# Kernel optimization log

Measured on AMD Instinct MI355X. Metric: run time of the kernel, lower is better.

Reference implementation:

```python
import jax, jax.numpy as jnp
import numpy as np
import math

D_MODEL = 1024
NUM_HEADS = 16
D_K = D_MODEL // NUM_HEADS
THETA = 10000.0
BATCH = 2
SEQ = 2048


def setup_inputs() -> dict:
    key = jax.random.key(0)
    k = jax.random.split(key, 6)
    scale = 1.0 / math.sqrt(D_MODEL)
    in_features = jax.random.normal(k[0], (BATCH, SEQ, D_MODEL), dtype=jnp.float32)
    token_positions = jnp.sort(
        jax.random.randint(k[1], (BATCH, SEQ), 0, SEQ), axis=-1
    ).astype(jnp.int32)
    q_proj_weight = jax.random.normal(k[2], (D_MODEL, D_MODEL), dtype=jnp.float32) * scale
    k_proj_weight = jax.random.normal(k[3], (D_MODEL, D_MODEL), dtype=jnp.float32) * scale
    v_proj_weight = jax.random.normal(k[4], (D_MODEL, D_MODEL), dtype=jnp.float32) * scale
    o_proj_weight = jax.random.normal(k[5], (D_MODEL, D_MODEL), dtype=jnp.float32) * scale
    return {
        "in_features": in_features,
        "token_positions": token_positions,
        "q_proj_weight": q_proj_weight,
        "k_proj_weight": k_proj_weight,
        "v_proj_weight": v_proj_weight,
        "o_proj_weight": o_proj_weight,
    }


def _apply_rope(x, positions):
    # x: [b, h, s, d_k]; positions: [b, s]
    freqs = 1.0 / (THETA ** (jnp.arange(0, D_K, 2, dtype=jnp.float32) / D_K))  # [d_k/2]
    angles = positions[:, None, :, None].astype(jnp.float32) * freqs  # [b,1,s,d_k/2]
    cos, sin = jnp.cos(angles), jnp.sin(angles)
    x1 = x[..., 0::2]
    x2 = x[..., 1::2]
    x1r = x1 * cos - x2 * sin
    x2r = x1 * sin + x2 * cos
    # interleave pairs back: stack on new last axis then flatten
    return jnp.stack([x1r, x2r], axis=-1).reshape(x.shape)


def reference(in_features, token_positions, q_proj_weight, k_proj_weight,
              v_proj_weight, o_proj_weight):
    b, s, _ = in_features.shape
    Q = jnp.einsum('bsi,di->bsd', in_features, q_proj_weight)
    K = jnp.einsum('bsi,di->bsd', in_features, k_proj_weight)
    V = jnp.einsum('bsi,di->bsd', in_features, v_proj_weight)
    # split heads: [b, h, s, d_k]
    def split(x):
        return x.reshape(b, s, NUM_HEADS, D_K).transpose(0, 2, 1, 3)
    Q, K, V = split(Q), split(K), split(V)
    Q = _apply_rope(Q, token_positions)
    K = _apply_rope(K, token_positions)
    scores = jnp.einsum('bhqd,bhkd->bhqk', Q, K) / math.sqrt(D_K)
    causal = jnp.tril(jnp.ones((s, s), dtype=bool))  # allowed positions
    scores = jnp.where(causal[None, None], scores, -jnp.inf)
    weights = jax.nn.softmax(scores, axis=-1)
    head_out = jnp.einsum('bhqk,bhkd->bhqd', weights, V)
    combined = head_out.transpose(0, 2, 1, 3).reshape(b, s, D_MODEL)
    return jnp.einsum('bsd,od->bso', combined, o_proj_weight)
```

## Files before the change

kernel.cpp:

```cpp
#include <hip/hip_runtime.h>
#include <hip/hip_bf16.h>
#include <stdint.h>

#define DMODEL 1024
#define NH 16
#define DKH 64
#define BB 2
#define SS 2048
#define MTOT (BB*SS)

#define TP 136

using f32x4  = __attribute__((ext_vector_type(4))) float;
using bf16x8 = __attribute__((ext_vector_type(8))) __bf16;

#define GLL(g, l) __builtin_amdgcn_global_load_lds( \
    (const __attribute__((address_space(1))) unsigned int*)(g), \
    (__attribute__((address_space(3))) unsigned int*)(l), 16, 0, 0)

__device__ __forceinline__ unsigned short f2bf(float f) {
  union { float f; uint32_t u; } v; v.f = f;
  uint32_t r = v.u + 0x7FFFu + ((v.u >> 16) & 1u);
  return (unsigned short)(r >> 16);
}

__global__ __launch_bounds__(256) void cvt_all(
    const float* __restrict__ X,
    const float* __restrict__ w0, const float* __restrict__ w1,
    const float* __restrict__ w2, const float* __restrict__ w3,
    unsigned short* __restrict__ Xb,
    unsigned short* __restrict__ Wb)
{
  const int bid = blockIdx.x;
  const float* src;
  unsigned short* dst;
  int i;
  if (bid < 2048) {
    src = X; dst = Xb; i = bid * 256 + threadIdx.x;
  } else {
    int t = bid - 2048;
    int z = t >> 9;
    src = (z == 0) ? w0 : (z == 1) ? w1 : (z == 2) ? w2 : w3;
    dst = Wb + (size_t)z * DMODEL * DMODEL;
    i = (t & 511) * 256 + threadIdx.x;
  }
  const float4* s4 = (const float4*)src;
  float4 a = s4[2*i], b = s4[2*i+1];
  uint4 o;
  o.x = (uint32_t)f2bf(a.x) | ((uint32_t)f2bf(a.y) << 16);
  o.y = (uint32_t)f2bf(a.z) | ((uint32_t)f2bf(a.w) << 16);
  o.z = (uint32_t)f2bf(b.x) | ((uint32_t)f2bf(b.y) << 16);
  o.w = (uint32_t)f2bf(b.z) | ((uint32_t)f2bf(b.w) << 16);
  *(uint4*)(dst + (size_t)i * 8) = o;
}

template<int MI, int NI, int KU>
__device__ __forceinline__ void gemm_pipe(
    const unsigned short* __restrict__ A,
    const unsigned short* __restrict__ Bw,
    int m0, int n0, int K,
    unsigned short* As, unsigned short* Bs,
    f32x4 (&acc)[MI][NI])
{
  const int BKT = 32 * KU;
  const int BMl = MI * 32;
  const int BNl = NI * 32;
  const int tid = threadIdx.x;
  const int lane = tid & 63;
  const int w = tid >> 6;
  const int wr = w >> 1, wc = w & 1;
  const int lrow = lane & 15;
  const int g = lane >> 4;

  const f32x4 fzero = {0.f, 0.f, 0.f, 0.f};
  #pragma unroll
  for (int i = 0; i < MI; ++i)
    #pragma unroll
    for (int j = 0; j < NI; ++j)
      acc[i][j] = fzero;

  const int nk = K / BKT;

  const unsigned short* aSrc[(MI * KU) / 2];
  const unsigned short* bSrc[(NI * KU) / 2];
  int aLds[(MI * KU) / 2], bLds[(NI * KU) / 2];
  #pragma unroll
  for (int c = 0; c < (MI * KU) / 2; ++c) {
    int i = tid + c * 256;
    int row, sc;
    if constexpr (KU == 1) { row = i >> 2; sc = (i & 3) ^ ((row >> 1) & 3); }
    else                   { row = i >> 3; sc = (i & 7) ^ (row & 7); }
    aSrc[c] = A + (size_t)(m0 + row) * K + sc * 8;
    aLds[c] = i * 8;
  }
  #pragma unroll
  for (int c = 0; c < (NI * KU) / 2; ++c) {
    int i = tid + c * 256;
    int row, sc;
    if constexpr (KU == 1) { row = i >> 2; sc = (i & 3) ^ ((row >> 1) & 3); }
    else                   { row = i >> 3; sc = (i & 7) ^ (row & 7); }
    bSrc[c] = Bw + (size_t)(n0 + row) * K + sc * 8;
    bLds[c] = i * 8;
  }
  int aOff[KU][MI], bOff[KU][NI];
  #pragma unroll
  for (int u = 0; u < KU; ++u) {
    #pragma unroll
    for (int mi = 0; mi < MI; ++mi) {
      int row = wr * (MI * 16) + mi * 16 + lrow;
      int ch = (KU == 1) ? (g ^ ((row >> 1) & 3)) : ((g + 4 * u) ^ (row & 7));
      aOff[u][mi] = row * BKT + ch * 8;
    }
    #pragma unroll
    for (int ni = 0; ni < NI; ++ni) {
      int row = wc * (NI * 16) + ni * 16 + lrow;
      int ch = (KU == 1) ? (g ^ ((row >> 1) & 3)) : ((g + 4 * u) ^ (row & 7));
      bOff[u][ni] = row * BKT + ch * 8;
    }
  }

  auto STAGE = [&](int k0, int buf) {
    #pragma unroll
    for (int c = 0; c < (MI * KU) / 2; ++c)
      GLL(aSrc[c] + k0, As + buf * (BMl * BKT) + aLds[c]);
    #pragma unroll
    for (int c = 0; c < (NI * KU) / 2; ++c)
      GLL(bSrc[c] + k0, Bs + buf * (BNl * BKT) + bLds[c]);
  };

  STAGE(0, 0);
  __syncthreads();
  for (int t = 0; t < nk; ++t) {
    const int cur = t & 1;
    if (t + 1 < nk) STAGE((t + 1) * BKT, cur ^ 1);

    const unsigned short* Ab = As + cur * (BMl * BKT);
    const unsigned short* Bb = Bs + cur * (BNl * BKT);
    #pragma unroll
    for (int u = 0; u < KU; ++u) {
      bf16x8 af[MI], bfr[NI];
      #pragma unroll
      for (int mi = 0; mi < MI; ++mi)
        af[mi] = *(const bf16x8*)(Ab + aOff[u][mi]);
      #pragma unroll
      for (int ni = 0; ni < NI; ++ni)
        bfr[ni] = *(const bf16x8*)(Bb + bOff[u][ni]);
      #pragma unroll
      for (int mi = 0; mi < MI; ++mi)
        #pragma unroll
        for (int ni = 0; ni < NI; ++ni)
          acc[mi][ni] = __builtin_amdgcn_mfma_f32_16x16x32_bf16(af[mi], bfr[ni], acc[mi][ni], 0, 0, 0);
    }

    __syncthreads();
  }
}

__global__ __launch_bounds__(256) void gemm_qkv(
    const unsigned short* __restrict__ Xb,
    const unsigned short* __restrict__ Wf,
    const int* __restrict__ tpos,
    unsigned short* __restrict__ Qh,
    unsigned short* __restrict__ Kh,
    unsigned short* __restrict__ Vt)
{
  __shared__ __align__(16) unsigned char smraw[65536];
  unsigned short* sm = (unsigned short*)smraw;
  unsigned short* As = sm;
  unsigned short* Bs = sm + 2 * 128 * 64;

  const int m0 = blockIdx.x * 128;
  const int n0 = blockIdx.y * 128;
  const int z  = n0 >> 10;
  const int nloc = n0 & 1023;

  f32x4 acc[4][4];
  gemm_pipe<4, 4, 2>(Xb, Wf, m0, n0, DMODEL, As, Bs, acc);

  const int tid  = threadIdx.x;
  const int lane = tid & 63;
  const int w    = tid >> 6;
  const int wr   = w >> 1, wc = w & 1;
  const int cb   = lane & 15, rb = (lane >> 4) * 4;

  if (z < 2) {
    #pragma unroll
    for (int mi = 0; mi < 4; ++mi)
      #pragma unroll
      for (int ni = 0; ni < 4; ++ni)
        #pragma unroll
        for (int r = 0; r < 4; ++r)
          sm[(wr * 64 + mi * 16 + rb + r) * TP + wc * 64 + ni * 16 + cb] = f2bf(acc[mi][ni][r]);
  } else {
    #pragma unroll
    for (int mi = 0; mi < 4; ++mi)
      #pragma unroll
      for (int ni = 0; ni < 4; ++ni)
        #pragma unroll
        for (int r = 0; r < 4; ++r)
          sm[(wc * 64 + ni * 16 + cb) * TP + wr * 64 + mi * 16 + rb + r] = f2bf(acc[mi][ni][r]);
  }
  __syncthreads();

  const int b = m0 >> 11;
  const float l2t = 13.28771237954945f / 32.0f;
  const float qsc = (z == 0) ? 0.18033688011112042f : 1.0f;

  if (z < 2) {
    unsigned short* dst = (z == 0) ? Qh : Kh;
    #pragma unroll
    for (int p = 0; p < 8; ++p) {
      const int m_l = p * 16 + (tid >> 4);
      const int ck  = tid & 15;
      bf16x8 vals = *(const bf16x8*)(sm + m_l * TP + ck * 8);
      const int m = m0 + m_l, s = m & (SS - 1);
      const int pos = tpos[m];
      const int n = nloc + ck * 8, h = n >> 6, dh = n & 63;
      union { unsigned short u[8]; uint4 v; } ov;
      #pragma unroll
      for (int e = 0; e < 4; ++e) {
        float x1 = (float)vals[2 * e], x2 = (float)vals[2 * e + 1];
        int j = (dh >> 1) + e;
        float ang = (float)pos * exp2f(-(float)j * l2t);
        float sn, cs;
        __sincosf(ang, &sn, &cs);
        sn *= qsc; cs *= qsc;
        ov.u[2 * e]     = f2bf(x1 * cs - x2 * sn);
        ov.u[2 * e + 1] = f2bf(x1 * sn + x2 * cs);
      }
      *(uint4*)(dst + ((size_t)(b * NH + h) * SS + s) * DKH + dh) = ov.v;
    }
  } else {
    #pragma unroll
    for (int p = 0; p < 8; ++p) {
      const int n_l = p * 16 + (tid >> 4);
      const int ck  = tid & 15;
      bf16x8 vals = *(const bf16x8*)(sm + n_l * TP + ck * 8);
      const int n = nloc + n_l, h = n >> 6, dh = n & 63;
      const int m = m0 + ck * 8, s = m & (SS - 1);
      *(bf16x8*)(Vt + ((size_t)(b * NH + h) * DKH + dh) * SS + s) = vals;
    }
  }
}

__global__ __launch_bounds__(256) void attn(
    const unsigned short* __restrict__ Qh,
    const unsigned short* __restrict__ Kh,
    const unsigned short* __restrict__ Vt,
    unsigned short* __restrict__ comb)
{
  __shared__ unsigned short Ks[2][128 * 64];
  __shared__ unsigned short Vs[2][64 * 128];
  __shared__ unsigned short Ps[4][32 * 64];

  const int idx = blockIdx.x;
  const int x = idx & 7;
  const int o = idx >> 3;
  const int bh = x * 4 + (o & 3);
  const int j = o >> 2;
  const int qt = ((j & 7) << 1) | (j >> 3);

  const int tid = threadIdx.x, lane = tid & 63, w = tid >> 6;
  const int lc = lane & 15, lh = lane >> 4;

  const unsigned short* kb = Kh + (size_t)bh * SS * DKH;
  const unsigned short* vb = Vt + (size_t)bh * DKH * SS;
  const int b = bh >> 4, h = bh & 15;
  const f32x4 fzero = {0.f, 0.f, 0.f, 0.f};
  const int Q0 = qt * 128;

  auto STAGE = [&](int t, int buf) {
    const int kv0 = t * 128;
    #pragma unroll
    for (int c = 0; c < 4; ++c) {
      int i = tid + c * 256;
      int row = i >> 3, pc = i & 7;
      int sc = pc ^ (row & 7);
      GLL(kb + (size_t)(kv0 + row) * DKH + sc * 8, &Ks[buf][i * 8]);
    }
    #pragma unroll
    for (int c = 0; c < 4; ++c) {
      int i = tid + c * 256;
      int row = i >> 4, cc = i & 15;
      int sc = cc ^ (row & 7);
      GLL(vb + (size_t)row * SS + kv0 + sc * 8, &Vs[buf][i * 8]);
    }
  };

  bf16x8 qf[2][2];
  #pragma unroll
  for (int qg = 0; qg < 2; ++qg) {
    const unsigned short* Qb = Qh + ((size_t)bh * SS + Q0 + w * 32 + qg * 16 + lc) * DKH;
    qf[qg][0] = *(const bf16x8*)(Qb + lh * 8);
    qf[qg][1] = *(const bf16x8*)(Qb + lh * 8 + 32);
  }

  f32x4 oacc[2][4];
  #pragma unroll
  for (int qg = 0; qg < 2; ++qg)
    #pragma unroll
    for (int i = 0; i < 4; ++i) oacc[qg][i] = fzero;
  float lsum[2] = {0.f, 0.f};
  unsigned short* psw = &Ps[w][0];

  auto QK = [&](int cur, int hh, f32x4 (&sacc)[2][4]) {
    __builtin_amdgcn_s_setprio(1);
    #pragma unroll
    for (int nf = 0; nf < 4; ++nf) {
      const int row = hh * 64 + nf * 16 + lc;
      bf16x8 kf0 = *(const bf16x8*)(&Ks[cur][row * 64 + ((lh) ^ (row & 7)) * 8]);
      bf16x8 kf1 = *(const bf16x8*)(&Ks[cur][row * 64 + ((lh + 4) ^ (row & 7)) * 8]);
      #pragma unroll
      for (int qg = 0; qg < 2; ++qg) {
        sacc[qg][nf] = __builtin_amdgcn_mfma_f32_16x16x32_bf16(kf0, qf[qg][0], fzero, 0, 0, 0);
        sacc[qg][nf] = __builtin_amdgcn_mfma_f32_16x16x32_bf16(kf1, qf[qg][1], sacc[qg][nf], 0, 0, 0);
      }
    }
    __builtin_amdgcn_s_setprio(0);
  };

  auto SM = [&](f32x4 (&sacc)[2][4], bool domask, int t, int hh) {
    #pragma unroll
    for (int qg = 0; qg < 2; ++qg) {
      float sv[4][4];
      if (domask) {
        const int kv0 = t * 128 + hh * 64;
        const int qlane = Q0 + w * 32 + qg * 16 + lc;
        #pragma unroll
        for (int nf = 0; nf < 4; ++nf)
          #pragma unroll
          for (int r = 0; r < 4; ++r) {
            float x2 = sacc[qg][nf][r];
            if ((kv0 + nf * 16 + lh * 4 + r) > qlane) x2 = -1e30f;
            sv[nf][r] = x2;
          }
      } else {
        #pragma unroll
        for (int nf = 0; nf < 4; ++nf)
          #pragma unroll
          for (int r = 0; r < 4; ++r)
            sv[nf][r] = sacc[qg][nf][r];
      }
      float rs = 0.f;
      #pragma unroll
      for (int nf = 0; nf < 4; ++nf)
        #pragma unroll
        for (int r = 0; r < 4; ++r) {
          float p = exp2f(sv[nf][r]);
          sv[nf][r] = p;
          rs += p;
        }
      lsum[qg] += rs;
      #pragma unroll
      for (int nf = 0; nf < 4; ++nf) {
        uint32_t u0, u1;
        asm("v_cvt_pk_bf16_f32 %0, %1, %2" : "=v"(u0) : "v"(sv[nf][0]), "v"(sv[nf][1]));
        asm("v_cvt_pk_bf16_f32 %0, %1, %2" : "=v"(u1) : "v"(sv[nf][2]), "v"(sv[nf][3]));
        int swz = (nf * 2 + (lh >> 1)) ^ (lc & 7);
        uint32_t* p = (uint32_t*)&psw[(qg * 16 + lc) * 64 + swz * 8 + (lh & 1) * 4];
        p[0] = u0; p[1] = u1;
      }
    }
  };

  auto PV = [&](int cur, int hh) {
    __builtin_amdgcn_s_setprio(1);
    #pragma unroll
    for (int c = 0; c < 2; ++c) {
      bf16x8 pf[2];
      #pragma unroll
      for (int qg = 0; qg < 2; ++qg)
        pf[qg] = *(const bf16x8*)(&psw[(qg * 16 + lc) * 64 + ((c * 4 + lh) ^ (lc & 7)) * 8]);
      #pragma unroll
      for (int df = 0; df < 4; ++df) {
        const int row = df * 16 + lc;
        bf16x8 vf = *(const bf16x8*)(&Vs[cur][row * 128 + ((hh * 8 + c * 4 + lh) ^ (row & 7)) * 8]);
        #pragma unroll
        for (int qg = 0; qg < 2; ++qg)
          oacc[qg][df] = __builtin_amdgcn_mfma_f32_16x16x32_bf16(pf[qg], vf, oacc[qg][df], 0, 0, 0);
      }
    }
    __builtin_amdgcn_s_setprio(0);
  };

  STAGE(0, 0);
  for (int t = 0; t < qt; ++t) {
    const int cur = t & 1;
    asm volatile("s_waitcnt vmcnt(0)" ::: "memory");
    __builtin_amdgcn_s_barrier();
    f32x4 sA[2][4], sB[2][4];
    QK(cur, 0, sA);
    QK(cur, 1, sB);
    STAGE(t + 1, cur ^ 1);
    SM(sA, false, t, 0);
    PV(cur, 0);
    SM(sB, false, t, 1);
    PV(cur, 1);
  }
  {
    const int cur = qt & 1;
    asm volatile("s_waitcnt vmcnt(0)" ::: "memory");
    __builtin_amdgcn_s_barrier();
    f32x4 sA[2][4], sB[2][4];
    QK(cur, 0, sA);
    QK(cur, 1, sB);
    SM(sA, true, qt, 0);
    PV(cur, 0);
    SM(sB, true, qt, 1);
    PV(cur, 1);
  }

  #pragma unroll
  for (int qg = 0; qg < 2; ++qg) {
    float ls0 = lsum[qg];
    ls0 += __shfl_xor(ls0, 16);
    ls0 += __shfl_xor(ls0, 32);
    #pragma unroll
    for (int r = 0; r < 4; ++r) {
      float ls = __shfl(ls0, lh * 4 + r);
      float inv = 1.f / ls;
      const int q = Q0 + w * 32 + qg * 16 + lh * 4 + r;
      #pragma unroll
      for (int df = 0; df < 4; ++df) {
        const int d = h * 64 + df * 16 + lc;
        comb[((size_t)(b * SS + q)) * DMODEL + d] = f2bf(oacc[qg][df][r] * inv);
      }
    }
  }
}

__global__ __launch_bounds__(256) void gemm_out(
    const unsigned short* __restrict__ Cb,
    const unsigned short* __restrict__ Wob,
    float* __restrict__ out)
{
  __shared__ __align__(16) unsigned char smraw[49152];
  unsigned short* As = (unsigned short*)smraw;
  unsigned short* Bs = (unsigned short*)smraw + 2 * 128 * 64;
  float* smf = (float*)smraw;

  const int m0 = blockIdx.x * 128, n0 = blockIdx.y * 64;
  f32x4 acc[4][2];
  gemm_pipe<4, 2, 2>(Cb, Wob, m0, n0, DMODEL, As, Bs, acc);

  const int tid  = threadIdx.x;
  const int lane = tid & 63;
  const int w    = tid >> 6;
  const int wr   = w >> 1, wc = w & 1;
  const int cb   = lane & 15, rb = (lane >> 4) * 4;

  #pragma unroll
  for (int mi = 0; mi < 4; ++mi)
    #pragma unroll
    for (int ni = 0; ni < 2; ++ni)
      #pragma unroll
      for (int r = 0; r < 4; ++r)
        smf[(wr * 64 + mi * 16 + rb + r) * 68 + wc * 32 + ni * 16 + cb] = acc[mi][ni][r];
  __syncthreads();

  #pragma unroll
  for (int p = 0; p < 8; ++p) {
    const int row = p * 16 + (tid >> 4);
    const int ck  = tid & 15;
    float4 vv = *(const float4*)(smf + row * 68 + ck * 4);
    *(float4*)(out + (size_t)(m0 + row) * DMODEL + n0 + ck * 4) = vv;
  }
}

extern "C" void kernel_launch(void* const* d_in, const int* in_sizes, int n_in,
                              void* d_out, int out_size, void* d_ws, size_t ws_size,
                              hipStream_t stream) {
  (void)in_sizes; (void)n_in; (void)out_size; (void)ws_size;
  const float* X    = (const float*)d_in[0];
  const int*   tpos = (const int*)d_in[1];
  const float* Wq   = (const float*)d_in[2];
  const float* Wk   = (const float*)d_in[3];
  const float* Wv   = (const float*)d_in[4];
  const float* Wo   = (const float*)d_in[5];
  float* out = (float*)d_out;

  uint8_t* ws = (uint8_t*)d_ws;
  const size_t SZ_X = (size_t)MTOT * DMODEL * 2;
  const size_t SZ_W = (size_t)DMODEL * DMODEL * 2;
  const size_t SZ_H = (size_t)BB * NH * SS * DKH * 2;
  unsigned short* Xb   = (unsigned short*)(ws);
  unsigned short* Wqb  = (unsigned short*)(ws + SZ_X);
  unsigned short* Wob  = (unsigned short*)(ws + SZ_X + 3 * SZ_W);
  unsigned short* Qh   = (unsigned short*)(ws + SZ_X + 4 * SZ_W);
  unsigned short* Kh   = (unsigned short*)(ws + SZ_X + 4 * SZ_W + SZ_H);
  unsigned short* Vt   = (unsigned short*)(ws + SZ_X + 4 * SZ_W + 2 * SZ_H);
  unsigned short* comb = Xb;

  cvt_all<<<dim3(4096), dim3(256), 0, stream>>>(X, Wq, Wk, Wv, Wo, Xb, Wqb);

  gemm_qkv<<<dim3(MTOT / 128, 24), dim3(256), 0, stream>>>(Xb, Wqb, tpos, Qh, Kh, Vt);
  attn<<<dim3(512), dim3(256), 0, stream>>>(Qh, Kh, Vt, comb);
  gemm_out<<<dim3(MTOT / 128, 16), dim3(256), 0, stream>>>(comb, Wob, out);
}
```

Before: 116.7 us.

## Split attention query tile across eight waves and reorder query-tile scheduling

The attention kernel now runs 512 threads per block. Each of the eight waves handles 16 query rows instead of 32, which halves per-wave accumulator registers and raises the number of waves sharing each staged K/V tile. The query-tile ordering changes from an interleaved permutation to a pattern that pairs short and long causal tiles (j for the first 8, 23-j after). The trade is more waves contending for LDS bandwidth, and each K fragment read from LDS now feeds only one MFMA rather than two.

```diff
diff --git a/kernel.cpp b/kernel.cpp
--- a/kernel.cpp
+++ b/kernel.cpp
@@ -243,7 +243,7 @@
   }
 }
 
-__global__ __launch_bounds__(256) void attn(
+__global__ __launch_bounds__(512) void attn(
     const unsigned short* __restrict__ Qh,
     const unsigned short* __restrict__ Kh,
     const unsigned short* __restrict__ Vt,
@@ -251,17 +251,18 @@
 {
   __shared__ unsigned short Ks[2][128 * 64];
   __shared__ unsigned short Vs[2][64 * 128];
-  __shared__ unsigned short Ps[4][32 * 64];
+  __shared__ unsigned short Ps[8][16 * 64];
 
   const int idx = blockIdx.x;
   const int x = idx & 7;
   const int o = idx >> 3;
   const int bh = x * 4 + (o & 3);
   const int j = o >> 2;
-  const int qt = ((j & 7) << 1) | (j >> 3);
+  const int qt = (j < 8) ? j : 23 - j;
 
   const int tid = threadIdx.x, lane = tid & 63, w = tid >> 6;
   const int lc = lane & 15, lh = lane >> 4;
+  const int wq = w >> 1, qg = w & 1;
 
   const unsigned short* kb = Kh + (size_t)bh * SS * DKH;
   const unsigned short* vb = Vt + (size_t)bh * DKH * SS;
@@ -272,94 +273,82 @@
   auto STAGE = [&](int t, int buf) {
     const int kv0 = t * 128;
     #pragma unroll
-    for (int c = 0; c < 4; ++c) {
-      int i = tid + c * 256;
+    for (int c = 0; c < 2; ++c) {
+      int i = tid + c * 512;
       int row = i >> 3, pc = i & 7;
       int sc = pc ^ (row & 7);
       GLL(kb + (size_t)(kv0 + row) * DKH + sc * 8, &Ks[buf][i * 8]);
     }
     #pragma unroll
-    for (int c = 0; c < 4; ++c) {
-      int i = tid + c * 256;
+    for (int c = 0; c < 2; ++c) {
+      int i = tid + c * 512;
       int row = i >> 4, cc = i & 15;
       int sc = cc ^ (row & 7);
       GLL(vb + (size_t)row * SS + kv0 + sc * 8, &Vs[buf][i * 8]);
     }
   };
 
-  bf16x8 qf[2][2];
-  #pragma unroll
-  for (int qg = 0; qg < 2; ++qg) {
-    const unsigned short* Qb = Qh + ((size_t)bh * SS + Q0 + w * 32 + qg * 16 + lc) * DKH;
-    qf[qg][0] = *(const bf16x8*)(Qb + lh * 8);
-    qf[qg][1] = *(const bf16x8*)(Qb + lh * 8 + 32);
-  }
-
-  f32x4 oacc[2][4];
-  #pragma unroll
-  for (int qg = 0; qg < 2; ++qg)
-    #pragma unroll
-    for (int i = 0; i < 4; ++i) oacc[qg][i] = fzero;
-  float lsum[2] = {0.f, 0.f};
+  const unsigned short* Qb = Qh + ((size_t)bh * SS + Q0 + wq * 32 + qg * 16 + lc) * DKH;
+  bf16x8 qf0 = *(const bf16x8*)(Qb + lh * 8);
+  bf16x8 qf1 = *(const bf16x8*)(Qb + lh * 8 + 32);
+
+  f32x4 oacc[4];
+  #pragma unroll
+  for (int i = 0; i < 4; ++i) oacc[i] = fzero;
+  float lsum = 0.f;
   unsigned short* psw = &Ps[w][0];
 
-  auto QK = [&](int cur, int hh, f32x4 (&sacc)[2][4]) {
+  auto QK = [&](int cur, int hh, f32x4 (&sacc)[4]) {
     __builtin_amdgcn_s_setprio(1);
     #pragma unroll
     for (int nf = 0; nf < 4; ++nf) {
       const int row = hh * 64 + nf * 16 + lc;
       bf16x8 kf0 = *(const bf16x8*)(&Ks[cur][row * 64 + ((lh) ^ (row & 7)) * 8]);
       bf16x8 kf1 = *(const bf16x8*)(&Ks[cur][row * 64 + ((lh + 4) ^ (row & 7)) * 8]);
-      #pragma unroll
-      for (int qg = 0; qg < 2; ++qg) {
-        sacc[qg][nf] = __builtin_amdgcn_mfma_f32_16x16x32_bf16(kf0, qf[qg][0], fzero, 0, 0, 0);
-        sacc[qg][nf] = __builtin_amdgcn_mfma_f32_16x16x32_bf16(kf1, qf[qg][1], sacc[qg][nf], 0, 0, 0);
-      }
+      sacc[nf] = __builtin_amdgcn_mfma_f32_16x16x32_bf16(kf0, qf0, fzero, 0, 0, 0);
+      sacc[nf] = __builtin_amdgcn_mfma_f32_16x16x32_bf16(kf1, qf1, sacc[nf], 0, 0, 0);
     }
     __builtin_amdgcn_s_setprio(0);
   };
 
-  auto SM = [&](f32x4 (&sacc)[2][4], bool domask, int t, int hh) {
-    #pragma unroll
-    for (int qg = 0; qg < 2; ++qg) {
-      float sv[4][4];
-      if (domask) {
-        const int kv0 = t * 128 + hh * 64;
-        const int qlane = Q0 + w * 32 + qg * 16 + lc;
-        #pragma unroll
-        for (int nf = 0; nf < 4; ++nf)
-          #pragma unroll
-          for (int r = 0; r < 4; ++r) {
-            float x2 = sacc[qg][nf][r];
-            if ((kv0 + nf * 16 + lh * 4 + r) > qlane) x2 = -1e30f;
-            sv[nf][r] = x2;
-          }
-      } else {
-        #pragma unroll
-        for (int nf = 0; nf < 4; ++nf)
-          #pragma unroll
-          for (int r = 0; r < 4; ++r)
-            sv[nf][r] = sacc[qg][nf][r];
-      }
-      float rs = 0.f;
+  auto SM = [&](f32x4 (&sacc)[4], bool domask, int t, int hh) {
+    float sv[4][4];
+    if (domask) {
+      const int kv0 = t * 128 + hh * 64;
+      const int qlane = Q0 + wq * 32 + qg * 16 + lc;
       #pragma unroll
       for (int nf = 0; nf < 4; ++nf)
         #pragma unroll
         for (int r = 0; r < 4; ++r) {
-          float p = exp2f(sv[nf][r]);
-          sv[nf][r] = p;
-          rs += p;
+          float x2 = sacc[nf][r];
+          if ((kv0 + nf * 16 + lh * 4 + r) > qlane) x2 = -1e30f;
+          sv[nf][r] = x2;
         }
-      lsum[qg] += rs;
-      #pragma unroll
-      for (int nf = 0; nf < 4; ++nf) {
-        uint32_t u0, u1;
-        asm("v_cvt_pk_bf16_f32 %0, %1, %2" : "=v"(u0) : "v"(sv[nf][0]), "v"(sv[nf][1]));
-        asm("v_cvt_pk_bf16_f32 %0, %1, %2" : "=v"(u1) : "v"(sv[nf][2]), "v"(sv[nf][3]));
-        int swz = (nf * 2 + (lh >> 1)) ^ (lc & 7);
-        uint32_t* p = (uint32_t*)&psw[(qg * 16 + lc) * 64 + swz * 8 + (lh & 1) * 4];
-        p[0] = u0; p[1] = u1;
+    } else {
+      #pragma unroll
+      for (int nf = 0; nf < 4; ++nf)
+        #pragma unroll
+        for (int r = 0; r < 4; ++r)
+          sv[nf][r] = sacc[nf][r];
+    }
+    float rs = 0.f;
+    #pragma unroll
+    for (int nf = 0; nf < 4; ++nf)
+      #pragma unroll
+      for (int r = 0; r < 4; ++r) {
+        float p = exp2f(sv[nf][r]);
+        sv[nf][r] = p;
+        rs += p;
       }
+    lsum += rs;
+    #pragma unroll
+    for (int nf = 0; nf < 4; ++nf) {
+      uint32_t u0, u1;
+      asm("v_cvt_pk_bf16_f32 %0, %1, %2" : "=v"(u0) : "v"(sv[nf][0]), "v"(sv[nf][1]));
+      asm("v_cvt_pk_bf16_f32 %0, %1, %2" : "=v"(u1) : "v"(sv[nf][2]), "v"(sv[nf][3]));
+      int swz = (nf * 2 + (lh >> 1)) ^ (lc & 7);
+      uint32_t* p = (uint32_t*)&psw[lc * 64 + swz * 8 + (lh & 1) * 4];
+      p[0] = u0; p[1] = u1;
     }
   };
 
@@ -367,17 +356,12 @@
     __builtin_amdgcn_s_setprio(1);
     #pragma unroll
     for (int c = 0; c < 2; ++c) {
-      bf16x8 pf[2];
-      #pragma unroll
-      for (int qg = 0; qg < 2; ++qg)
-        pf[qg] = *(const bf16x8*)(&psw[(qg * 16 + lc) * 64 + ((c * 4 + lh) ^ (lc & 7)) * 8]);
+      bf16x8 pf = *(const bf16x8*)(&psw[lc * 64 + ((c * 4 + lh) ^ (lc & 7)) * 8]);
       #pragma unroll
       for (int df = 0; df < 4; ++df) {
         const int row = df * 16 + lc;
         bf16x8 vf = *(const bf16x8*)(&Vs[cur][row * 128 + ((hh * 8 + c * 4 + lh) ^ (row & 7)) * 8]);
-        #pragma unroll
-        for (int qg = 0; qg < 2; ++qg)
-          oacc[qg][df] = __builtin_amdgcn_mfma_f32_16x16x32_bf16(pf[qg], vf, oacc[qg][df], 0, 0, 0);
+        oacc[df] = __builtin_amdgcn_mfma_f32_16x16x32_bf16(pf, vf, oacc[df], 0, 0, 0);
       }
     }
     __builtin_amdgcn_s_setprio(0);
@@ -388,7 +372,7 @@
     const int cur = t & 1;
     asm volatile("s_waitcnt vmcnt(0)" ::: "memory");
     __builtin_amdgcn_s_barrier();
-    f32x4 sA[2][4], sB[2][4];
+    f32x4 sA[4], sB[4];
     QK(cur, 0, sA);
     QK(cur, 1, sB);
     STAGE(t + 1, cur ^ 1);
@@ -401,7 +385,7 @@
     const int cur = qt & 1;
     asm volatile("s_waitcnt vmcnt(0)" ::: "memory");
     __builtin_amdgcn_s_barrier();
-    f32x4 sA[2][4], sB[2][4];
+    f32x4 sA[4], sB[4];
     QK(cur, 0, sA);
     QK(cur, 1, sB);
     SM(sA, true, qt, 0);
@@ -410,21 +394,17 @@
     PV(cur, 1);
   }
 
-  #pragma unroll
-  for (int qg = 0; qg < 2; ++qg) {
-    float ls0 = lsum[qg];
-    ls0 += __shfl_xor(ls0, 16);
-    ls0 += __shfl_xor(ls0, 32);
-    #pragma unroll
-    for (int r = 0; r < 4; ++r) {
-      float ls = __shfl(ls0, lh * 4 + r);
-      float inv = 1.f / ls;
-      const int q = Q0 + w * 32 + qg * 16 + lh * 4 + r;
-      #pragma unroll
-      for (int df = 0; df < 4; ++df) {
-        const int d = h * 64 + df * 16 + lc;
-        comb[((size_t)(b * SS + q)) * DMODEL + d] = f2bf(oacc[qg][df][r] * inv);
-      }
+  lsum += __shfl_xor(lsum, 16);
+  lsum += __shfl_xor(lsum, 32);
+  #pragma unroll
+  for (int r = 0; r < 4; ++r) {
+    float ls = __shfl(lsum, lh * 4 + r);
+    float inv = 1.f / ls;
+    const int q = Q0 + wq * 32 + qg * 16 + lh * 4 + r;
+    #pragma unroll
+    for (int df = 0; df < 4; ++df) {
+      const int d = h * 64 + df * 16 + lc;
+      comb[((size_t)(b * SS + q)) * DMODEL + d] = f2bf(oacc[df][r] * inv);
     }
   }
 }
@@ -494,6 +474,6 @@
   cvt_all<<<dim3(4096), dim3(256), 0, stream>>>(X, Wq, Wk, Wv, Wo, Xb, Wqb);
 
   gemm_qkv<<<dim3(MTOT / 128, 24), dim3(256), 0, stream>>>(Xb, Wqb, tpos, Qh, Kh, Vt);
-  attn<<<dim3(512), dim3(256), 0, stream>>>(Qh, Kh, Vt, comb);
+  attn<<<dim3(512), dim3(512), 0, stream>>>(Qh, Kh, Vt, comb);
   gemm_out<<<dim3(MTOT / 128, 16), dim3(256), 0, stream>>>(comb, Wob, out);
 }
```

Result: faster. 97.04 us (median of 2 runs) (-16.9%).
